# Kernel optimization log

Hardware: AMD Instinct MI355X
Metric: run time of the kernel (lower is better)

## Reference

```python
import jax, jax.numpy as jnp
import numpy as np

N = 100000
E = 1000000
IN_F, HID, NCLS = 128, 128, 40
EPS = 1e-5


def _gconv(h, src, dst, W, b):
    # DGL GraphConv with norm='both', allow_zero_in_degree=True (degrees clamped to >=1).
    ones = jnp.ones(src.shape, jnp.float32)
    dout = jnp.clip(jax.ops.segment_sum(ones, src, num_segments=N), 1.0)   # out-degree of src nodes
    din = jnp.clip(jax.ops.segment_sum(ones, dst, num_segments=N), 1.0)    # in-degree of dst nodes
    x = (h * jax.lax.rsqrt(dout)[:, None]) @ W            # [N, out] matmul-first (linear commutes with sum-aggregation)
    y = jax.ops.segment_sum(x[src], dst, num_segments=N)  # SpMM: scatter-add over edges
    y = y * jax.lax.rsqrt(din)[:, None]
    return y + b if b is not None else y


def _bn(h, gamma, beta):
    # BatchNorm1d training-mode math over the node dimension (biased variance).
    m = jnp.mean(h, axis=0)
    v = jnp.mean(jnp.square(h - m), axis=0)
    return (h - m) * jax.lax.rsqrt(v + EPS) * gamma + beta


def setup_inputs() -> dict:
    key = jax.random.key(0)
    ks = jax.random.split(key, 16)
    feat = jax.random.normal(ks[0], (N, IN_F), jnp.float32)
    src0 = jax.random.randint(ks[1], (E,), 0, N, jnp.int32)
    dst0 = jax.random.randint(ks[2], (E,), 0, N, jnp.int32)
    src1 = jax.random.randint(ks[3], (E,), 0, N, jnp.int32)
    dst1 = jax.random.randint(ks[4], (E,), 0, N, jnp.int32)
    order_attn = jax.random.uniform(ks[5], (2,), jnp.float32)
    s = lambda d_in, d_out: 1.0 / np.sqrt(d_in)
    W0 = jax.random.uniform(ks[6], (IN_F, HID), jnp.float32, -s(IN_F, HID), s(IN_F, HID))
    W1 = jax.random.uniform(ks[7], (HID, HID), jnp.float32, -s(HID, HID), s(HID, HID))
    W2 = jax.random.uniform(ks[8], (HID, NCLS), jnp.float32, -s(HID, NCLS), s(HID, NCLS))
    b2 = jnp.zeros((NCLS,), jnp.float32)
    L0 = jax.random.uniform(ks[9], (IN_F, HID), jnp.float32, -s(IN_F, HID), s(IN_F, HID))
    L1 = jax.random.uniform(ks[10], (HID, HID), jnp.float32, -s(HID, HID), s(HID, HID))
    L2 = jax.random.uniform(ks[11], (HID, NCLS), jnp.float32, -s(HID, NCLS), s(HID, NCLS))
    gamma0 = jnp.ones((HID,), jnp.float32); beta0 = jnp.zeros((HID,), jnp.float32)
    gamma1 = jnp.ones((HID,), jnp.float32); beta1 = jnp.zeros((HID,), jnp.float32)
    return dict(feat=feat, src0=src0, dst0=dst0, src1=src1, dst1=dst1, order_attn=order_attn,
                W0=W0, W1=W1, W2=W2, b2=b2, L0=L0, L1=L1, L2=L2,
                gamma0=gamma0, beta0=beta0, gamma1=gamma1, beta1=beta1)


def reference(feat, src0, dst0, src1, dst1, order_attn, W0, W1, W2, b2, L0, L1, L2,
              gamma0, beta0, gamma1, beta1):
    # Multi-graph path (len(graph)==2, n_layers==3, use_linear=True); dropout = identity (eval).
    h = feat
    # layer 0: order_attn-weighted combination of two adjacency variants
    conv1 = _gconv(h, src0, dst0, W0, None)
    conv2 = _gconv(h, src1, dst1, W0, None)
    conv = order_attn[0] * conv1 + order_attn[1] * conv2
    h = conv + h @ L0
    h = jax.nn.relu(_bn(h, gamma0, beta0))
    # layer 1 (convs[-2]) on graph[0]
    h = _gconv(h, src0, dst0, W1, None) + h @ L1
    h = jax.nn.relu(_bn(h, gamma1, beta1))
    # layer 2 (convs[-1]) on graph[0], with bias
    h = _gconv(h, src0, dst0, W2, b2) + h @ L2
    return h
```

## Files before the change

### kernel.cpp

```cpp
#include <hip/hip_runtime.h>
#include <math.h>

#define N_NODES 100000
#define N_EDGES 1000000
#define F 128
#define NC 40
#define BN_EPS 1e-5f
#define CH 32
#define EC (N_EDGES / CH)
#define WIN0 65536
#define NB1 (N_NODES - WIN0)
#define PROW (N_NODES / 4)
#define CSU 68
#define GB 1563

typedef unsigned int uint;
typedef unsigned short ushort;
typedef __attribute__((ext_vector_type(8))) short vbf8;
typedef __attribute__((ext_vector_type(4))) float vf4;

__device__ __forceinline__ float bf_lo(uint v) { return __uint_as_float(v << 16); }
__device__ __forceinline__ float bf_hi(uint v) { return __uint_as_float(v & 0xffff0000u); }
__device__ __forceinline__ ushort f2bf(float f) {
  uint u = __float_as_uint(f);
  u = u + 0x7fffu + ((u >> 16) & 1u);
  return (ushort)(u >> 16);
}
__device__ __forceinline__ uint pk2(float a, float b) {
  return (uint)f2bf(a) | ((uint)f2bf(b) << 16);
}

__global__ __launch_bounds__(256) void hist_count_k(
    const int* __restrict__ s0, const int* __restrict__ d0,
    const int* __restrict__ s1, const int* __restrict__ d1,
    unsigned* __restrict__ partial) {
  __shared__ unsigned bins[16384];
  int c = blockIdx.x, w = blockIdx.y, a = blockIdx.z;
  const int* keys = (a == 0) ? s0 : (a == 1) ? d0 : (a == 2) ? s1 : d1;
  int base = w * WIN0;
  int nb = w ? NB1 : WIN0;
  int nwords = nb >> 2;
  int t = threadIdx.x;
  for (int i = t; i < nwords; i += 256) bins[i] = 0;
  __syncthreads();
  int e0 = c * EC;
  for (int e = e0 + t; e < e0 + EC; e += 256) {
    int b = keys[e] - base;
    if ((unsigned)b < (unsigned)nb)
      atomicAdd(&bins[b >> 2], 1u << ((b & 3) * 8));
  }
  __syncthreads();
  unsigned* dst = partial + (size_t)(a * CH + c) * PROW + (w ? (WIN0 >> 2) : 0);
  for (int i = t; i < nwords; i += 256) dst[i] = bins[i];
}

__global__ __launch_bounds__(256) void deg_reduce_k(
    unsigned* __restrict__ partial, float* __restrict__ rs4, ushort* __restrict__ rsO01u,
    int* __restrict__ degIn0, int* __restrict__ degIn1) {
  int word = blockIdx.x * 256 + threadIdx.x;
  if (word >= PROW) return;
  int a = blockIdx.y;
  bool din = (a == 1) || (a == 3);
  unsigned r0 = 0, r1 = 0, r2 = 0, r3 = 0;
  unsigned* rowp = partial + (size_t)a * CH * PROW + word;
  for (int c = 0; c < CH; ++c) {
    unsigned* p = rowp + (size_t)c * PROW;
    unsigned v = *p;
    if (din) *p = r0 | (r1 << 8) | (r2 << 16) | (r3 << 24);
    r0 += v & 255u; r1 += (v >> 8) & 255u; r2 += (v >> 16) & 255u; r3 += (v >> 24) & 255u;
  }
  int b = word * 4;
  float4 r;
  r.x = rsqrtf((float)max(r0, 1u));
  r.y = rsqrtf((float)max(r1, 1u));
  r.z = rsqrtf((float)max(r2, 1u));
  r.w = rsqrtf((float)max(r3, 1u));
  *(float4*)&rs4[(size_t)a * N_NODES + b] = r;
  if (a == 0) {
    rsO01u[2 * (b + 0)] = f2bf(r.x); rsO01u[2 * (b + 1)] = f2bf(r.y);
    rsO01u[2 * (b + 2)] = f2bf(r.z); rsO01u[2 * (b + 3)] = f2bf(r.w);
  }
  if (a == 2) {
    rsO01u[2 * (b + 0) + 1] = f2bf(r.x); rsO01u[2 * (b + 1) + 1] = f2bf(r.y);
    rsO01u[2 * (b + 2) + 1] = f2bf(r.z); rsO01u[2 * (b + 3) + 1] = f2bf(r.w);
  }
  if (a == 1) { degIn0[b] = r0; degIn0[b + 1] = r1; degIn0[b + 2] = r2; degIn0[b + 3] = r3; }
  if (a == 3) { degIn1[b] = r0; degIn1[b + 1] = r1; degIn1[b + 2] = r2; degIn1[b + 3] = r3; }
}

__global__ void scan_local_k(const int* __restrict__ cnt0, const int* __restrict__ cnt1,
                             int* __restrict__ out0, int* __restrict__ out1,
                             int* __restrict__ bsum) {
  __shared__ int lds[256];
  const int* cnt = blockIdx.y ? cnt1 : cnt0;
  int* out = blockIdx.y ? out1 : out0;
  int base = blockIdx.x * 2048;
  int t = threadIdx.x;
  int v[8];
  int s = 0;
#pragma unroll
  for (int j = 0; j < 8; ++j) {
    int idx = base + t * 8 + j;
    v[j] = (idx < N_NODES) ? cnt[idx] : 0;
    s += v[j];
  }
  lds[t] = s;
  __syncthreads();
  for (int off = 1; off < 256; off <<= 1) {
    int x = (t >= off) ? lds[t - off] : 0;
    __syncthreads();
    lds[t] += x;
    __syncthreads();
  }
  int excl = lds[t] - s;
  if (t == 255) bsum[blockIdx.y * 64 + blockIdx.x] = lds[255];
  int run = excl;
#pragma unroll
  for (int j = 0; j < 8; ++j) {
    int idx = base + t * 8 + j;
    if (idx < N_NODES) out[idx] = run;
    run += v[j];
  }
}

__global__ void scan_top_k(int* bsum, int nb) {
  int w = threadIdx.x >> 6, t = threadIdx.x & 63;
  int* b = bsum + w * 64;
  int orig = (t < nb) ? b[t] : 0;
  int v = orig;
  for (int off = 1; off < 64; off <<= 1) {
    int u = __shfl_up(v, off);
    if (t >= off) v += u;
  }
  if (t < nb) b[t] = v - orig;
}

__global__ void scan_apply_k(int* __restrict__ rp0, int* __restrict__ rp1,
                             const int* __restrict__ bsum) {
  int* rp = blockIdx.y ? rp1 : rp0;
  const int* bs = bsum + blockIdx.y * 64;
  int i = blockIdx.x * 256 + threadIdx.x;
  if (i < N_NODES) rp[i] += bs[i >> 11];
  if (i == 0) rp[N_NODES] = N_EDGES;
}

__global__ __launch_bounds__(256) void csr_fill2_k(
    const int* __restrict__ src0, const int* __restrict__ dst0, const int* __restrict__ rp0g,
    int* __restrict__ csr0g,
    const int* __restrict__ src1, const int* __restrict__ dst1, const int* __restrict__ rp1g,
    int* __restrict__ csr1g, const unsigned* __restrict__ partial) {
  __shared__ unsigned bins[16384];
  int c = blockIdx.x, w = blockIdx.y, g = blockIdx.z;
  const int* src = g ? src1 : src0;
  const int* dst = g ? dst1 : dst0;
  const int* rp = g ? rp1g : rp0g;
  int* csr = g ? csr1g : csr0g;
  int aIdx = g ? 3 : 1;
  int base = w * WIN0;
  int nb = w ? NB1 : WIN0;
  int nwords = nb >> 2;
  const unsigned* sp = partial + (size_t)(aIdx * CH + c) * PROW + (w ? (WIN0 >> 2) : 0);
  int t = threadIdx.x;
  for (int i = t; i < nwords; i += 256) bins[i] = sp[i];
  __syncthreads();
  int e0 = c * EC;
  for (int e = e0 + t; e < e0 + EC; e += 256) {
    int d = dst[e];
    int b = d - base;
    if ((unsigned)b < (unsigned)nb) {
      int sh = (b & 3) * 8;
      unsigned old = atomicAdd(&bins[b >> 2], 1u << sh);
      int off = (old >> sh) & 255;
      csr[rp[d] + off] = src[e];
    }
  }
}

__global__ __launch_bounds__(256) void pack_all_k(
    const float* __restrict__ x, uint* __restrict__ y,
    const float* __restrict__ Wa, const float* __restrict__ Wb,
    const float* __restrict__ Wc, const float* __restrict__ Wd,
    ushort* __restrict__ pk) {
  int b = blockIdx.x;
  int t = threadIdx.x;
  if (b < 1024) {
    size_t total = (size_t)N_NODES * F / 8;
    for (size_t idx = b * 256 + t; idx < total; idx += (size_t)1024 * 256) {
      float4 v1 = ((const float4*)x)[idx * 2];
      float4 v2 = ((const float4*)x)[idx * 2 + 1];
      uint4 o;
      o.x = pk2(v1.x, v1.y);
      o.y = pk2(v1.z, v1.w);
      o.z = pk2(v2.x, v2.y);
      o.w = pk2(v2.z, v2.w);
      ((uint4*)y)[idx] = o;
    }
  } else {
    int bb = b - 1024;
    int m = bb >> 3;
    int idx = (bb & 7) * 256 + t;
    const float* W = (m == 0) ? Wa : (m == 1) ? Wb : (m == 2) ? Wc : Wd;
    int lane = idx & 63;
    int nt = (idx >> 6) & 7;
    int ks = idx >> 9;
    int j = (lane & 15) + nt * 16;
    int kb = (lane >> 4) * 8 + ks * 32;
    ushort v[8];
#pragma unroll
    for (int q = 0; q < 8; ++q) v[q] = f2bf(W[(size_t)(kb + q) * F + j]);
    *(uint4*)(pk + (size_t)m * 16384 + (size_t)idx * 8) = *(uint4*)v;
  }
}

__global__ void st_part_k(const float* __restrict__ stm, float* __restrict__ stp, int ncopies) {
  int b = blockIdx.x, t = threadIdx.x;
  int lo = b * 25, hi = min(ncopies, lo + 25);
  float s = 0.f;
  for (int k = lo; k < hi; ++k) s += stm[(size_t)k * 256 + t];
  stp[b * 256 + t] = s;
}

__global__ void st_final_k(const float* __restrict__ stp, float* __restrict__ st) {
  int t = threadIdx.x;
  float s = 0.f;
#pragma unroll
  for (int k = 0; k < 64; ++k) s += stp[k * 256 + t];
  st[t] = s;
}

__device__ __forceinline__ void acc8(uint4 v, float c, float* a) {
  a[0] = fmaf(bf_lo(v.x), c, a[0]); a[1] = fmaf(bf_hi(v.x), c, a[1]);
  a[2] = fmaf(bf_lo(v.y), c, a[2]); a[3] = fmaf(bf_hi(v.y), c, a[3]);
  a[4] = fmaf(bf_lo(v.z), c, a[4]); a[5] = fmaf(bf_hi(v.z), c, a[5]);
  a[6] = fmaf(bf_lo(v.w), c, a[6]); a[7] = fmaf(bf_hi(v.w), c, a[7]);
}

__device__ __forceinline__ void gather_run(const int* __restrict__ p, int n, float w,
                                           const float* __restrict__ rsO,
                                           const uint4* __restrict__ xr, int l, float* a) {
  int e = 0;
  for (; e + 3 < n; e += 4) {
    int s0 = p[e], s1 = p[e + 1], s2 = p[e + 2], s3 = p[e + 3];
    float c0 = w * rsO[s0], c1 = w * rsO[s1];
    float c2 = w * rsO[s2], c3 = w * rsO[s3];
    uint4 v0 = xr[(size_t)s0 * 16 + l];
    uint4 v1 = xr[(size_t)s1 * 16 + l];
    uint4 v2 = xr[(size_t)s2 * 16 + l];
    uint4 v3 = xr[(size_t)s3 * 16 + l];
    acc8(v0, c0, a); acc8(v1, c1, a); acc8(v2, c2, a); acc8(v3, c3, a);
  }
  for (; e < n; ++e) {
    int s = p[e];
    float c = w * rsO[s];
    uint4 v = xr[(size_t)s * 16 + l];
    acc8(v, c, a);
  }
}

__global__ __launch_bounds__(256) void gather_dual_q_k(
    const uint* __restrict__ xbf, const float* __restrict__ attn,
    const float* __restrict__ rsO0f, const float* __restrict__ rsO1f,
    const float* __restrict__ rsI0, const int* __restrict__ rp0, const int* __restrict__ csr0,
    const float* __restrict__ rsI1, const int* __restrict__ rp1, const int* __restrict__ csr1,
    uint* __restrict__ outbf) {
  int node = blockIdx.x * 16 + (threadIdx.x >> 4);
  int l = threadIdx.x & 15;
  int b0 = rp0[node], n0 = rp0[node + 1] - b0;
  int b1 = rp1[node], n1 = rp1[node + 1] - b1;
  float w0 = attn[0] * rsI0[node];
  float w1 = attn[1] * rsI1[node];
  const uint4* xr = (const uint4*)xbf;
  float a[8] = {0.f, 0.f, 0.f, 0.f, 0.f, 0.f, 0.f, 0.f};
  gather_run(csr0 + b0, n0, w0, rsO0f, xr, l, a);
  gather_run(csr1 + b1, n1, w1, rsO1f, xr, l, a);
  uint4 o;
  o.x = pk2(a[0], a[1]); o.y = pk2(a[2], a[3]);
  o.z = pk2(a[4], a[5]); o.w = pk2(a[6], a[7]);
  ((uint4*)outbf)[(size_t)node * 16 + l] = o;
}

__device__ __forceinline__ void accbn(uint4 v, float c, const float* sc, const float* sh,
                                      float* a) {
  a[0] = fmaf(fmaxf(fmaf(bf_lo(v.x), sc[0], sh[0]), 0.f), c, a[0]);
  a[1] = fmaf(fmaxf(fmaf(bf_hi(v.x), sc[1], sh[1]), 0.f), c, a[1]);
  a[2] = fmaf(fmaxf(fmaf(bf_lo(v.y), sc[2], sh[2]), 0.f), c, a[2]);
  a[3] = fmaf(fmaxf(fmaf(bf_hi(v.y), sc[3], sh[3]), 0.f), c, a[3]);
  a[4] = fmaf(fmaxf(fmaf(bf_lo(v.z), sc[4], sh[4]), 0.f), c, a[4]);
  a[5] = fmaf(fmaxf(fmaf(bf_hi(v.z), sc[5], sh[5]), 0.f), c, a[5]);
  a[6] = fmaf(fmaxf(fmaf(bf_lo(v.w), sc[6], sh[6]), 0.f), c, a[6]);
  a[7] = fmaf(fmaxf(fmaf(bf_hi(v.w), sc[7], sh[7]), 0.f), c, a[7]);
}

__global__ __launch_bounds__(256) void gather_bn_q_k(
    const uint* __restrict__ xbf, const float* __restrict__ st,
    const float* __restrict__ gamma, const float* __restrict__ beta,
    const float* __restrict__ rsO,
    const float* __restrict__ rsI, const int* __restrict__ rp, const int* __restrict__ csr,
    uint* __restrict__ outbf) {
  int node = blockIdx.x * 16 + (threadIdx.x >> 4);
  int l = threadIdx.x & 15;
  float sc[8], sh[8];
#pragma unroll
  for (int j = 0; j < 8; ++j) {
    int c = 8 * l + j;
    float m = st[c] * (1.f / (float)N_NODES);
    float v = st[128 + c] * (1.f / (float)N_NODES) - m * m;
    float s = gamma[c] * rsqrtf(fmaxf(v, 0.f) + BN_EPS);
    sc[j] = s;
    sh[j] = beta[c] - m * s;
  }
  int b0 = rp[node], T = rp[node + 1] - b0;
  const int* p = csr + b0;
  const uint4* xr = (const uint4*)xbf;
  float a[8] = {0.f, 0.f, 0.f, 0.f, 0.f, 0.f, 0.f, 0.f};
  int e = 0;
  for (; e + 1 < T; e += 2) {
    int s0 = p[e], s1 = p[e + 1];
    float c0 = rsO[s0], c1 = rsO[s1];
    uint4 v0 = xr[(size_t)s0 * 16 + l];
    uint4 v1 = xr[(size_t)s1 * 16 + l];
    accbn(v0, c0, sc, sh, a);
    accbn(v1, c1, sc, sh, a);
  }
  if (e < T) {
    int s0 = p[e];
    float c0 = rsO[s0];
    uint4 v0 = xr[(size_t)s0 * 16 + l];
    accbn(v0, c0, sc, sh, a);
  }
  float sd = rsI[node];
  uint4 o;
  o.x = pk2(a[0] * sd, a[1] * sd); o.y = pk2(a[2] * sd, a[3] * sd);
  o.z = pk2(a[4] * sd, a[5] * sd); o.w = pk2(a[6] * sd, a[7] * sd);
  ((uint4*)outbf)[(size_t)node * 16 + l] = o;
}

__global__ void gather40_add_k(const uint* __restrict__ x2bf, const float* __restrict__ rsI,
                               const int* __restrict__ rp, const int* __restrict__ csr,
                               float* __restrict__ out) {
  int node = (blockIdx.x * 256 + threadIdx.x) >> 5;
  int lane = threadIdx.x & 31;
  if (node >= N_NODES || lane >= 20) return;
  float l = 0.f, h = 0.f;
  int e = rp[node], end = rp[node + 1];
  for (; e + 3 < end; e += 4) {
    int sA = csr[e], sB = csr[e + 1], sC = csr[e + 2], sD = csr[e + 3];
    uint vA = x2bf[(size_t)sA * 20 + lane];
    uint vB = x2bf[(size_t)sB * 20 + lane];
    uint vC = x2bf[(size_t)sC * 20 + lane];
    uint vD = x2bf[(size_t)sD * 20 + lane];
    l += (bf_lo(vA) + bf_lo(vB)) + (bf_lo(vC) + bf_lo(vD));
    h += (bf_hi(vA) + bf_hi(vB)) + (bf_hi(vC) + bf_hi(vD));
  }
  for (; e < end; ++e) {
    uint vA = x2bf[(size_t)csr[e] * 20 + lane];
    l += bf_lo(vA);
    h += bf_hi(vA);
  }
  float sd = rsI[node];
  float2 p = *(float2*)(out + (size_t)node * NC + lane * 2);
  *(float2*)(out + (size_t)node * NC + lane * 2) = make_float2(p.x + l * sd, p.y + h * sd);
}

__global__ __launch_bounds__(256) void gemm_mfma_k(
    const ushort* __restrict__ A1, const ushort* __restrict__ A2,
    const ushort* __restrict__ pkA, const ushort* __restrict__ pkB,
    float* __restrict__ stm, ushort* __restrict__ Cb) {
  __shared__ uint Cl[64 * CSU];
  __shared__ float sst[256];
  int t = threadIdx.x;
  sst[t] = 0.f;
  __syncthreads();
  int wave = t >> 6, lane = t & 63;
  int kgrp = lane >> 4, lrow = lane & 15;
  int arow = blockIdx.x * 64 + wave * 16 + lrow;
  bool rok = arow < N_NODES;
  const vbf8* a1p = (const vbf8*)(A1 + (size_t)(rok ? arow : 0) * F);
  const vbf8* a2p = (const vbf8*)(A2 + (size_t)(rok ? arow : 0) * F);
  const vbf8* wap = (const vbf8*)pkA + lane;
  const vbf8* wbp = (const vbf8*)pkB + lane;
  vbf8 zero = {0, 0, 0, 0, 0, 0, 0, 0};
  vf4 acc[8];
#pragma unroll
  for (int i = 0; i < 8; ++i) acc[i] = (vf4){0.f, 0.f, 0.f, 0.f};
#pragma unroll
  for (int ks = 0; ks < 4; ++ks) {
    vbf8 a1 = rok ? a1p[ks * 4 + kgrp] : zero;
    vbf8 a2 = rok ? a2p[ks * 4 + kgrp] : zero;
#pragma unroll
    for (int nt = 0; nt < 8; ++nt)
      acc[nt] = __builtin_amdgcn_mfma_f32_16x16x32_bf16(a1, wap[(ks * 8 + nt) * 64], acc[nt], 0, 0, 0);
#pragma unroll
    for (int nt = 0; nt < 8; ++nt)
      acc[nt] = __builtin_amdgcn_mfma_f32_16x16x32_bf16(a2, wbp[(ks * 8 + nt) * 64], acc[nt], 0, 0, 0);
  }
  int row_l = wave * 16 + kgrp * 4;
#pragma unroll
  for (int nt = 0; nt < 8; ++nt) {
#pragma unroll
    for (int r = 0; r < 4; ++r) {
      float w = acc[nt][r];
      float o = __shfl_xor(w, 1);
      if ((lrow & 1) == 0) Cl[(row_l + r) * CSU + nt * 8 + (lrow >> 1)] = pk2(w, o);
    }
  }
#pragma unroll
  for (int nt = 0; nt < 8; ++nt) {
    float s = acc[nt][0] + acc[nt][1] + acc[nt][2] + acc[nt][3];
    float q = acc[nt][0] * acc[nt][0] + acc[nt][1] * acc[nt][1] +
              acc[nt][2] * acc[nt][2] + acc[nt][3] * acc[nt][3];
    s += __shfl_xor(s, 16); q += __shfl_xor(q, 16);
    s += __shfl_xor(s, 32); q += __shfl_xor(q, 32);
    if (lane < 16) {
      atomicAdd(&sst[nt * 16 + lane], s);
      atomicAdd(&sst[128 + nt * 16 + lane], q);
    }
  }
  __syncthreads();
#pragma unroll
  for (int i = 0; i < 4; ++i) {
    int u = t + 256 * i;
    int row = u >> 4, seg = (u & 15) * 4;
    int grow = blockIdx.x * 64 + row;
    if (grow < N_NODES)
      *(uint4*)((uint*)Cb + (size_t)grow * 64 + seg) = *(uint4*)&Cl[row * CSU + seg];
  }
  stm[(size_t)blockIdx.x * 256 + t] = sst[t];
}

__global__ __launch_bounds__(256) void gemm_mfma_bn_k(
    const ushort* __restrict__ A1, const ushort* __restrict__ A2,
    const float* __restrict__ stin, const float* __restrict__ gamma,
    const float* __restrict__ beta,
    const ushort* __restrict__ pkA, const ushort* __restrict__ pkB,
    float* __restrict__ stm, ushort* __restrict__ Cb) {
  __shared__ uint Cl[64 * CSU];
  __shared__ float sst[256];
  __shared__ float scl[128], shl[128];
  int t = threadIdx.x;
  sst[t] = 0.f;
  if (t < 128) {
    float m = stin[t] * (1.f / (float)N_NODES);
    float v = stin[128 + t] * (1.f / (float)N_NODES) - m * m;
    float s = gamma[t] * rsqrtf(fmaxf(v, 0.f) + BN_EPS);
    scl[t] = s;
    shl[t] = beta[t] - m * s;
  }
  __syncthreads();
  int wave = t >> 6, lane = t & 63;
  int kgrp = lane >> 4, lrow = lane & 15;
  int arow = blockIdx.x * 64 + wave * 16 + lrow;
  bool rok = arow < N_NODES;
  const vbf8* a1p = (const vbf8*)(A1 + (size_t)(rok ? arow : 0) * F);
  const vbf8* a2p = (const vbf8*)(A2 + (size_t)(rok ? arow : 0) * F);
  const vbf8* wap = (const vbf8*)pkA + lane;
  const vbf8* wbp = (const vbf8*)pkB + lane;
  vbf8 zero = {0, 0, 0, 0, 0, 0, 0, 0};
  vf4 acc[8];
#pragma unroll
  for (int i = 0; i < 8; ++i) acc[i] = (vf4){0.f, 0.f, 0.f, 0.f};
#pragma unroll
  for (int ks = 0; ks < 4; ++ks) {
    vbf8 a1 = rok ? a1p[ks * 4 + kgrp] : zero;
    vbf8 a2 = zero;
    if (rok) {
      vbf8 a2r = a2p[ks * 4 + kgrp];
      const float* scp = &scl[ks * 32 + kgrp * 8];
      const float* shp = &shl[ks * 32 + kgrp * 8];
      ushort o[8];
#pragma unroll
      for (int q = 0; q < 8; ++q) {
        float f = __uint_as_float(((uint)(ushort)a2r[q]) << 16);
        f = fmaxf(fmaf(f, scp[q], shp[q]), 0.f);
        o[q] = f2bf(f);
      }
      a2 = *(vbf8*)o;
    }
#pragma unroll
    for (int nt = 0; nt < 8; ++nt)
      acc[nt] = __builtin_amdgcn_mfma_f32_16x16x32_bf16(a1, wap[(ks * 8 + nt) * 64], acc[nt], 0, 0, 0);
#pragma unroll
    for (int nt = 0; nt < 8; ++nt)
      acc[nt] = __builtin_amdgcn_mfma_f32_16x16x32_bf16(a2, wbp[(ks * 8 + nt) * 64], acc[nt], 0, 0, 0);
  }
  int row_l = wave * 16 + kgrp * 4;
#pragma unroll
  for (int nt = 0; nt < 8; ++nt) {
#pragma unroll
    for (int r = 0; r < 4; ++r) {
      float w = acc[nt][r];
      float o = __shfl_xor(w, 1);
      if ((lrow & 1) == 0) Cl[(row_l + r) * CSU + nt * 8 + (lrow >> 1)] = pk2(w, o);
    }
  }
#pragma unroll
  for (int nt = 0; nt < 8; ++nt) {
    float s = acc[nt][0] + acc[nt][1] + acc[nt][2] + acc[nt][3];
    float q = acc[nt][0] * acc[nt][0] + acc[nt][1] * acc[nt][1] +
              acc[nt][2] * acc[nt][2] + acc[nt][3] * acc[nt][3];
    s += __shfl_xor(s, 16); q += __shfl_xor(q, 16);
    s += __shfl_xor(s, 32); q += __shfl_xor(q, 32);
    if (lane < 16) {
      atomicAdd(&sst[nt * 16 + lane], s);
      atomicAdd(&sst[128 + nt * 16 + lane], q);
    }
  }
  __syncthreads();
#pragma unroll
  for (int i = 0; i < 4; ++i) {
    int u = t + 256 * i;
    int row = u >> 4, seg = (u & 15) * 4;
    int grow = blockIdx.x * 64 + row;
    if (grow < N_NODES)
      *(uint4*)((uint*)Cb + (size_t)grow * 64 + seg) = *(uint4*)&Cl[row * CSU + seg];
  }
  stm[(size_t)blockIdx.x * 256 + t] = sst[t];
}

__global__ __launch_bounds__(256) void gemm40_dual_k(
    const uint* __restrict__ h1b, const float* __restrict__ st,
    const float* __restrict__ gamma, const float* __restrict__ beta,
    const float* __restrict__ W2, const float* __restrict__ L2, const float* __restrict__ bias,
    const float* __restrict__ rsO, uint* __restrict__ x2bf, float* __restrict__ outp) {
  __shared__ float Alds[25 * 128];
  __shared__ float Wl[128 * NC];
  __shared__ float Ll[128 * NC];
  __shared__ float scl[128], shl[128];
  int t = threadIdx.x;
  int r0 = blockIdx.x * 25;
  if (t < 128) {
    float m = st[t] / (float)N_NODES;
    float v = st[128 + t] / (float)N_NODES - m * m;
    float s = gamma[t] * rsqrtf(fmaxf(v, 0.f) + BN_EPS);
    scl[t] = s;
    shl[t] = beta[t] - m * s;
  }
  __syncthreads();
#pragma unroll
  for (int p = 0; p < 4; ++p) {
    int flat = t * 4 + p * 1024;
    if (flat < 25 * 128) {
      int lrr = flat >> 7, k = flat & 127;
      int row = r0 + lrr;
      float4 v = make_float4(0.f, 0.f, 0.f, 0.f);
      if (row < N_NODES) {
        uint2 u = *(const uint2*)(h1b + (size_t)row * 64 + (k >> 1));
        v = make_float4(bf_lo(u.x), bf_hi(u.x), bf_lo(u.y), bf_hi(u.y));
      }
      float4 scv = *(float4*)&scl[k];
      float4 shv = *(float4*)&shl[k];
      v.x = fmaxf(fmaf(v.x, scv.x, shv.x), 0.f);
      v.y = fmaxf(fmaf(v.y, scv.y, shv.y), 0.f);
      v.z = fmaxf(fmaf(v.z, scv.z, shv.z), 0.f);
      v.w = fmaxf(fmaf(v.w, scv.w, shv.w), 0.f);
      *(float4*)&Alds[flat] = v;
    }
  }
#pragma unroll
  for (int p = 0; p < 5; ++p) {
    int flat = t * 4 + p * 1024;
    if (flat < 128 * NC) {
      *(float4*)&Wl[flat] = *(const float4*)(W2 + flat);
      *(float4*)&Ll[flat] = *(const float4*)(L2 + flat);
    }
  }
  __syncthreads();
  if (t < 250) {
    int lrr = t / 10, cg = t % 10;
    float w0 = 0.f, w1 = 0.f, w2 = 0.f, w3 = 0.f;
    float l0 = 0.f, l1 = 0.f, l2 = 0.f, l3 = 0.f;
#pragma unroll 8
    for (int k = 0; k < 128; ++k) {
      float a = Alds[lrr * 128 + k];
      float4 w = *(float4*)&Wl[k * NC + cg * 4];
      float4 l = *(float4*)&Ll[k * NC + cg * 4];
      w0 = fmaf(a, w.x, w0); w1 = fmaf(a, w.y, w1);
      w2 = fmaf(a, w.z, w2); w3 = fmaf(a, w.w, w3);
      l0 = fmaf(a, l.x, l0); l1 = fmaf(a, l.y, l1);
      l2 = fmaf(a, l.z, l2); l3 = fmaf(a, l.w, l3);
    }
    int row = r0 + lrr;
    if (row < N_NODES) {
      float s = rsO[row];
      uint2 xo = make_uint2(pk2(w0 * s, w1 * s), pk2(w2 * s, w3 * s));
      *(uint2*)(x2bf + (size_t)row * 20 + cg * 2) = xo;
      float4 bv = *(const float4*)(bias + cg * 4);
      float4 oo = make_float4(l0 + bv.x, l1 + bv.y, l2 + bv.z, l3 + bv.w);
      *(float4*)(outp + (size_t)row * NC + cg * 4) = oo;
    }
  }
}

extern "C" void kernel_launch(void* const* d_in, const int* in_sizes, int n_in,
                              void* d_out, int out_size, void* d_ws, size_t ws_size,
                              hipStream_t stream) {
  const float* feat = (const float*)d_in[0];
  const int* src0 = (const int*)d_in[1];
  const int* dst0 = (const int*)d_in[2];
  const int* src1 = (const int*)d_in[3];
  const int* dst1 = (const int*)d_in[4];
  const float* attn = (const float*)d_in[5];
  const float* W0 = (const float*)d_in[6];
  const float* W1 = (const float*)d_in[7];
  const float* W2 = (const float*)d_in[8];
  const float* b2 = (const float*)d_in[9];
  const float* L0 = (const float*)d_in[10];
  const float* L1 = (const float*)d_in[11];
  const float* L2 = (const float*)d_in[12];
  const float* gamma0 = (const float*)d_in[13];
  const float* beta0 = (const float*)d_in[14];
  const float* gamma1 = (const float*)d_in[15];
  const float* beta1 = (const float*)d_in[16];
  float* out = (float*)d_out;

  char* base = (char*)d_ws;
  size_t off = 0;
  auto alloc = [&](size_t bytes) -> void* {
    void* p = base + off;
    off += (bytes + 255) & ~(size_t)255;
    return p;
  };
  unsigned* partial = (unsigned*)alloc((size_t)4 * CH * PROW * 4);
  float* rs4 = (float*)alloc(4 * (size_t)N_NODES * 4);
  uint* rsO01 = (uint*)alloc((size_t)N_NODES * 4);
  int* degIn0 = (int*)alloc(N_NODES * 4);
  int* degIn1 = (int*)alloc(N_NODES * 4);
  int* rp0 = (int*)alloc((N_NODES + 1) * 4);
  int* rp1 = (int*)alloc((N_NODES + 1) * 4);
  int* bsum = (int*)alloc(128 * 4);
  int* csr0 = (int*)alloc((size_t)N_EDGES * 4);
  int* csr1 = (int*)alloc((size_t)N_EDGES * 4);
  float* stm0 = (float*)alloc((size_t)GB * 256 * 4);
  float* stm1 = (float*)alloc((size_t)GB * 256 * 4);
  float* stp = (float*)alloc((size_t)64 * 256 * 4);
  float* st0 = (float*)alloc(256 * 4);
  float* st1 = (float*)alloc(256 * 4);
  ushort* wpk = (ushort*)alloc((size_t)4 * 16384 * 2);
  uint* featbf = (uint*)alloc((size_t)N_NODES * 64 * 4);
  uint* aggbf = (uint*)alloc((size_t)N_NODES * 64 * 4);
  uint* hrow = (uint*)alloc((size_t)N_NODES * 64 * 4);
  uint* g1buf = (uint*)alloc((size_t)N_NODES * 64 * 4);
  if (off > ws_size) return;

  uint* x2bf = featbf;

  float* rs_out0 = rs4;
  float* rs_in0 = rs4 + N_NODES;
  float* rs_out1 = rs4 + 2 * N_NODES;
  float* rs_in1 = rs4 + 3 * N_NODES;

  hist_count_k<<<dim3(CH, 2, 4), 256, 0, stream>>>(src0, dst0, src1, dst1, partial);
  deg_reduce_k<<<dim3((PROW + 255) / 256, 4), 256, 0, stream>>>(
      partial, rs4, (ushort*)rsO01, degIn0, degIn1);
  const int SCB = (N_NODES + 2047) / 2048;
  scan_local_k<<<dim3(SCB, 2), 256, 0, stream>>>(degIn0, degIn1, rp0, rp1, bsum);
  scan_top_k<<<1, 128, 0, stream>>>(bsum, SCB);
  scan_apply_k<<<dim3((N_NODES + 255) / 256, 2), 256, 0, stream>>>(rp0, rp1, bsum);
  csr_fill2_k<<<dim3(CH, 2, 2), 256, 0, stream>>>(src0, dst0, rp0, csr0,
                                                  src1, dst1, rp1, csr1, partial);

  pack_all_k<<<1056, 256, 0, stream>>>(feat, featbf, W0, L0, W1, L1, wpk);

  gather_dual_q_k<<<N_NODES / 16, 256, 0, stream>>>(featbf, attn, rs_out0, rs_out1,
                                                    rs_in0, rp0, csr0,
                                                    rs_in1, rp1, csr1, aggbf);
  gemm_mfma_k<<<GB, 256, 0, stream>>>((ushort*)aggbf, (ushort*)featbf, wpk, wpk + 16384,
                                      stm0, (ushort*)hrow);
  st_part_k<<<64, 256, 0, stream>>>(stm0, stp, GB);
  st_final_k<<<1, 256, 0, stream>>>(stp, st0);

  gather_bn_q_k<<<N_NODES / 16, 256, 0, stream>>>(hrow, st0, gamma0, beta0, rs_out0,
                                                  rs_in0, rp0, csr0, g1buf);
  gemm_mfma_bn_k<<<GB, 256, 0, stream>>>((ushort*)g1buf, (ushort*)hrow, st0, gamma0, beta0,
                                         wpk + 2 * 16384, wpk + 3 * 16384, stm1, (ushort*)hrow);
  st_part_k<<<64, 256, 0, stream>>>(stm1, stp, GB);
  st_final_k<<<1, 256, 0, stream>>>(stp, st1);

  gemm40_dual_k<<<(N_NODES + 24) / 25, 256, 0, stream>>>(hrow, st1, gamma1, beta1, W2, L2, b2,
                                                         rs_out0, x2bf, out);
  gather40_add_k<<<(N_NODES * 32 + 255) / 256, 256, 0, stream>>>(x2bf, rs_in0, rp0, csr0, out);
}
```

Baseline: 468.1 us.

## Split 128-wide gathers into eight 16-feature column slices across grid.x

The two 128-feature SpMM gather kernels now run over a 2D grid where blockIdx.x picks a 16-column slice and each node uses 4 lanes loading uint2, instead of 16 lanes loading uint4 over the full row. Blocks working on the same slice touch only a 3.2 MB portion of the feature matrix, so the random gathers are meant to hit in L2/MALL more often. The cost is that each node's CSR indices and degree scales are re-read eight times. The dual gather also reads the packed bf16 rsO01 out-degree scales instead of two fp32 arrays, which lowers coefficient precision slightly.

Result: slower. 721.4 us (+54.1%).

```diff
diff --git a/kernel.cpp b/kernel.cpp
--- a/kernel.cpp
+++ b/kernel.cpp
@@ -228,111 +228,136 @@
   st[t] = s;
 }
 
-__device__ __forceinline__ void acc8(uint4 v, float c, float* a) {
-  a[0] = fmaf(bf_lo(v.x), c, a[0]); a[1] = fmaf(bf_hi(v.x), c, a[1]);
-  a[2] = fmaf(bf_lo(v.y), c, a[2]); a[3] = fmaf(bf_hi(v.y), c, a[3]);
-  a[4] = fmaf(bf_lo(v.z), c, a[4]); a[5] = fmaf(bf_hi(v.z), c, a[5]);
-  a[6] = fmaf(bf_lo(v.w), c, a[6]); a[7] = fmaf(bf_hi(v.w), c, a[7]);
-}
-
-__device__ __forceinline__ void gather_run(const int* __restrict__ p, int n, float w,
-                                           const float* __restrict__ rsO,
-                                           const uint4* __restrict__ xr, int l, float* a) {
-  int e = 0;
-  for (; e + 3 < n; e += 4) {
-    int s0 = p[e], s1 = p[e + 1], s2 = p[e + 2], s3 = p[e + 3];
-    float c0 = w * rsO[s0], c1 = w * rsO[s1];
-    float c2 = w * rsO[s2], c3 = w * rsO[s3];
-    uint4 v0 = xr[(size_t)s0 * 16 + l];
-    uint4 v1 = xr[(size_t)s1 * 16 + l];
-    uint4 v2 = xr[(size_t)s2 * 16 + l];
-    uint4 v3 = xr[(size_t)s3 * 16 + l];
-    acc8(v0, c0, a); acc8(v1, c1, a); acc8(v2, c2, a); acc8(v3, c3, a);
-  }
-  for (; e < n; ++e) {
-    int s = p[e];
-    float c = w * rsO[s];
-    uint4 v = xr[(size_t)s * 16 + l];
-    acc8(v, c, a);
-  }
-}
-
-__global__ __launch_bounds__(256) void gather_dual_q_k(
+__global__ __launch_bounds__(256) void gather_dual_s_k(
     const uint* __restrict__ xbf, const float* __restrict__ attn,
-    const float* __restrict__ rsO0f, const float* __restrict__ rsO1f,
+    const uint* __restrict__ rsO01,
     const float* __restrict__ rsI0, const int* __restrict__ rp0, const int* __restrict__ csr0,
     const float* __restrict__ rsI1, const int* __restrict__ rp1, const int* __restrict__ csr1,
     uint* __restrict__ outbf) {
-  int node = blockIdx.x * 16 + (threadIdx.x >> 4);
-  int l = threadIdx.x & 15;
+  int s = blockIdx.x;
+  int node = blockIdx.y * 64 + (threadIdx.x >> 2);
+  int sl = threadIdx.x & 3;
+  if (node >= N_NODES) return;
+  const uint2* xc = (const uint2*)xbf + s * 4 + sl;
   int b0 = rp0[node], n0 = rp0[node + 1] - b0;
   int b1 = rp1[node], n1 = rp1[node + 1] - b1;
   float w0 = attn[0] * rsI0[node];
   float w1 = attn[1] * rsI1[node];
-  const uint4* xr = (const uint4*)xbf;
-  float a[8] = {0.f, 0.f, 0.f, 0.f, 0.f, 0.f, 0.f, 0.f};
-  gather_run(csr0 + b0, n0, w0, rsO0f, xr, l, a);
-  gather_run(csr1 + b1, n1, w1, rsO1f, xr, l, a);
-  uint4 o;
-  o.x = pk2(a[0], a[1]); o.y = pk2(a[2], a[3]);
-  o.z = pk2(a[4], a[5]); o.w = pk2(a[6], a[7]);
-  ((uint4*)outbf)[(size_t)node * 16 + l] = o;
-}
-
-__device__ __forceinline__ void accbn(uint4 v, float c, const float* sc, const float* sh,
-                                      float* a) {
-  a[0] = fmaf(fmaxf(fmaf(bf_lo(v.x), sc[0], sh[0]), 0.f), c, a[0]);
-  a[1] = fmaf(fmaxf(fmaf(bf_hi(v.x), sc[1], sh[1]), 0.f), c, a[1]);
-  a[2] = fmaf(fmaxf(fmaf(bf_lo(v.y), sc[2], sh[2]), 0.f), c, a[2]);
-  a[3] = fmaf(fmaxf(fmaf(bf_hi(v.y), sc[3], sh[3]), 0.f), c, a[3]);
-  a[4] = fmaf(fmaxf(fmaf(bf_lo(v.z), sc[4], sh[4]), 0.f), c, a[4]);
-  a[5] = fmaf(fmaxf(fmaf(bf_hi(v.z), sc[5], sh[5]), 0.f), c, a[5]);
-  a[6] = fmaf(fmaxf(fmaf(bf_lo(v.w), sc[6], sh[6]), 0.f), c, a[6]);
-  a[7] = fmaf(fmaxf(fmaf(bf_hi(v.w), sc[7], sh[7]), 0.f), c, a[7]);
-}
-
-__global__ __launch_bounds__(256) void gather_bn_q_k(
+  float a0 = 0.f, a1 = 0.f, a2 = 0.f, a3 = 0.f;
+  {
+    const int* p = csr0 + b0;
+    int e = 0;
+    for (; e + 3 < n0; e += 4) {
+      int s0 = p[e], s1 = p[e + 1], s2 = p[e + 2], s3 = p[e + 3];
+      float c0 = w0 * bf_lo(rsO01[s0]);
+      float c1 = w0 * bf_lo(rsO01[s1]);
+      float c2 = w0 * bf_lo(rsO01[s2]);
+      float c3 = w0 * bf_lo(rsO01[s3]);
+      uint2 v0 = xc[(size_t)s0 * 32];
+      uint2 v1 = xc[(size_t)s1 * 32];
+      uint2 v2 = xc[(size_t)s2 * 32];
+      uint2 v3 = xc[(size_t)s3 * 32];
+      a0 = fmaf(bf_lo(v0.x), c0, a0); a1 = fmaf(bf_hi(v0.x), c0, a1);
+      a2 = fmaf(bf_lo(v0.y), c0, a2); a3 = fmaf(bf_hi(v0.y), c0, a3);
+      a0 = fmaf(bf_lo(v1.x), c1, a0); a1 = fmaf(bf_hi(v1.x), c1, a1);
+      a2 = fmaf(bf_lo(v1.y), c1, a2); a3 = fmaf(bf_hi(v1.y), c1, a3);
+      a0 = fmaf(bf_lo(v2.x), c2, a0); a1 = fmaf(bf_hi(v2.x), c2, a1);
+      a2 = fmaf(bf_lo(v2.y), c2, a2); a3 = fmaf(bf_hi(v2.y), c2, a3);
+      a0 = fmaf(bf_lo(v3.x), c3, a0); a1 = fmaf(bf_hi(v3.x), c3, a1);
+      a2 = fmaf(bf_lo(v3.y), c3, a2); a3 = fmaf(bf_hi(v3.y), c3, a3);
+    }
+    for (; e < n0; ++e) {
+      int s0 = p[e];
+      float c0 = w0 * bf_lo(rsO01[s0]);
+      uint2 v0 = xc[(size_t)s0 * 32];
+      a0 = fmaf(bf_lo(v0.x), c0, a0); a1 = fmaf(bf_hi(v0.x), c0, a1);
+      a2 = fmaf(bf_lo(v0.y), c0, a2); a3 = fmaf(bf_hi(v0.y), c0, a3);
+    }
+  }
+  {
+    const int* p = csr1 + b1;
+    int e = 0;
+    for (; e + 3 < n1; e += 4) {
+      int s0 = p[e], s1 = p[e + 1], s2 = p[e + 2], s3 = p[e + 3];
+      float c0 = w1 * bf_hi(rsO01[s0]);
+      float c1 = w1 * bf_hi(rsO01[s1]);
+      float c2 = w1 * bf_hi(rsO01[s2]);
+      float c3 = w1 * bf_hi(rsO01[s3]);
+      uint2 v0 = xc[(size_t)s0 * 32];
+      uint2 v1 = xc[(size_t)s1 * 32];
+      uint2 v2 = xc[(size_t)s2 * 32];
+      uint2 v3 = xc[(size_t)s3 * 32];
+      a0 = fmaf(bf_lo(v0.x), c0, a0); a1 = fmaf(bf_hi(v0.x), c0, a1);
+      a2 = fmaf(bf_lo(v0.y), c0, a2); a3 = fmaf(bf_hi(v0.y), c0, a3);
+      a0 = fmaf(bf_lo(v1.x), c1, a0); a1 = fmaf(bf_hi(v1.x), c1, a1);
+      a2 = fmaf(bf_lo(v1.y), c1, a2); a3 = fmaf(bf_hi(v1.y), c1, a3);
+      a0 = fmaf(bf_lo(v2.x), c2, a0); a1 = fmaf(bf_hi(v2.x), c2, a1);
+      a2 = fmaf(bf_lo(v2.y), c2, a2); a3 = fmaf(bf_hi(v2.y), c2, a3);
+      a0 = fmaf(bf_lo(v3.x), c3, a0); a1 = fmaf(bf_hi(v3.x), c3, a1);
+      a2 = fmaf(bf_lo(v3.y), c3, a2); a3 = fmaf(bf_hi(v3.y), c3, a3);
+    }
+    for (; e < n1; ++e) {
+      int s0 = p[e];
+      float c0 = w1 * bf_hi(rsO01[s0]);
+      uint2 v0 = xc[(size_t)s0 * 32];
+      a0 = fmaf(bf_lo(v0.x), c0, a0); a1 = fmaf(bf_hi(v0.x), c0, a1);
+      a2 = fmaf(bf_lo(v0.y), c0, a2); a3 = fmaf(bf_hi(v0.y), c0, a3);
+    }
+  }
+  ((uint2*)outbf)[(size_t)node * 32 + s * 4 + sl] = make_uint2(pk2(a0, a1), pk2(a2, a3));
+}
+
+__global__ __launch_bounds__(256) void gather_bn_s_k(
     const uint* __restrict__ xbf, const float* __restrict__ st,
     const float* __restrict__ gamma, const float* __restrict__ beta,
     const float* __restrict__ rsO,
     const float* __restrict__ rsI, const int* __restrict__ rp, const int* __restrict__ csr,
     uint* __restrict__ outbf) {
-  int node = blockIdx.x * 16 + (threadIdx.x >> 4);
-  int l = threadIdx.x & 15;
-  float sc[8], sh[8];
-#pragma unroll
-  for (int j = 0; j < 8; ++j) {
-    int c = 8 * l + j;
+  int s = blockIdx.x;
+  int node = blockIdx.y * 64 + (threadIdx.x >> 2);
+  int sl = threadIdx.x & 3;
+  if (node >= N_NODES) return;
+  float sc[4], sh[4];
+#pragma unroll
+  for (int j = 0; j < 4; ++j) {
+    int c = s * 16 + sl * 4 + j;
     float m = st[c] * (1.f / (float)N_NODES);
     float v = st[128 + c] * (1.f / (float)N_NODES) - m * m;
-    float s = gamma[c] * rsqrtf(fmaxf(v, 0.f) + BN_EPS);
-    sc[j] = s;
-    sh[j] = beta[c] - m * s;
-  }
+    float g = gamma[c] * rsqrtf(fmaxf(v, 0.f) + BN_EPS);
+    sc[j] = g;
+    sh[j] = beta[c] - m * g;
+  }
+  const uint2* xc = (const uint2*)xbf + s * 4 + sl;
   int b0 = rp[node], T = rp[node + 1] - b0;
   const int* p = csr + b0;
-  const uint4* xr = (const uint4*)xbf;
-  float a[8] = {0.f, 0.f, 0.f, 0.f, 0.f, 0.f, 0.f, 0.f};
+  float a0 = 0.f, a1 = 0.f, a2 = 0.f, a3 = 0.f;
   int e = 0;
   for (; e + 1 < T; e += 2) {
     int s0 = p[e], s1 = p[e + 1];
     float c0 = rsO[s0], c1 = rsO[s1];
-    uint4 v0 = xr[(size_t)s0 * 16 + l];
-    uint4 v1 = xr[(size_t)s1 * 16 + l];
-    accbn(v0, c0, sc, sh, a);
-    accbn(v1, c1, sc, sh, a);
+    uint2 v0 = xc[(size_t)s0 * 32];
+    uint2 v1 = xc[(size_t)s1 * 32];
+    a0 = fmaf(fmaxf(fmaf(bf_lo(v0.x), sc[0], sh[0]), 0.f), c0, a0);
+    a1 = fmaf(fmaxf(fmaf(bf_hi(v0.x), sc[1], sh[1]), 0.f), c0, a1);
+    a2 = fmaf(fmaxf(fmaf(bf_lo(v0.y), sc[2], sh[2]), 0.f), c0, a2);
+    a3 = fmaf(fmaxf(fmaf(bf_hi(v0.y), sc[3], sh[3]), 0.f), c0, a3);
+    a0 = fmaf(fmaxf(fmaf(bf_lo(v1.x), sc[0], sh[0]), 0.f), c1, a0);
+    a1 = fmaf(fmaxf(fmaf(bf_hi(v1.x), sc[1], sh[1]), 0.f), c1, a1);
+    a2 = fmaf(fmaxf(fmaf(bf_lo(v1.y), sc[2], sh[2]), 0.f), c1, a2);
+    a3 = fmaf(fmaxf(fmaf(bf_hi(v1.y), sc[3], sh[3]), 0.f), c1, a3);
   }
   if (e < T) {
     int s0 = p[e];
     float c0 = rsO[s0];
-    uint4 v0 = xr[(size_t)s0 * 16 + l];
-    accbn(v0, c0, sc, sh, a);
+    uint2 v0 = xc[(size_t)s0 * 32];
+    a0 = fmaf(fmaxf(fmaf(bf_lo(v0.x), sc[0], sh[0]), 0.f), c0, a0);
+    a1 = fmaf(fmaxf(fmaf(bf_hi(v0.x), sc[1], sh[1]), 0.f), c0, a1);
+    a2 = fmaf(fmaxf(fmaf(bf_lo(v0.y), sc[2], sh[2]), 0.f), c0, a2);
+    a3 = fmaf(fmaxf(fmaf(bf_hi(v0.y), sc[3], sh[3]), 0.f), c0, a3);
   }
   float sd = rsI[node];
-  uint4 o;
-  o.x = pk2(a[0] * sd, a[1] * sd); o.y = pk2(a[2] * sd, a[3] * sd);
-  o.z = pk2(a[4] * sd, a[5] * sd); o.w = pk2(a[6] * sd, a[7] * sd);
-  ((uint4*)outbf)[(size_t)node * 16 + l] = o;
+  ((uint2*)outbf)[(size_t)node * 32 + s * 4 + sl] =
+      make_uint2(pk2(a0 * sd, a1 * sd), pk2(a2 * sd, a3 * sd));
 }
 
 __global__ void gather40_add_k(const uint* __restrict__ x2bf, const float* __restrict__ rsI,
@@ -661,7 +686,9 @@
 
   pack_all_k<<<1056, 256, 0, stream>>>(feat, featbf, W0, L0, W1, L1, wpk);
 
-  gather_dual_q_k<<<N_NODES / 16, 256, 0, stream>>>(featbf, attn, rs_out0, rs_out1,
+  const int GYB = (N_NODES + 63) / 64;
+
+  gather_dual_s_k<<<dim3(8, GYB), 256, 0, stream>>>(featbf, attn, rsO01,
                                                     rs_in0, rp0, csr0,
                                                     rs_in1, rp1, csr1, aggbf);
   gemm_mfma_k<<<GB, 256, 0, stream>>>((ushort*)aggbf, (ushort*)featbf, wpk, wpk + 16384,
@@ -669,7 +696,7 @@
   st_part_k<<<64, 256, 0, stream>>>(stm0, stp, GB);
   st_final_k<<<1, 256, 0, stream>>>(stp, st0);
 
-  gather_bn_q_k<<<N_NODES / 16, 256, 0, stream>>>(hrow, st0, gamma0, beta0, rs_out0,
+  gather_bn_s_k<<<dim3(8, GYB), 256, 0, stream>>>(hrow, st0, gamma0, beta0, rs_out0,
                                                   rs_in0, rp0, csr0, g1buf);
   gemm_mfma_bn_k<<<GB, 256, 0, stream>>>((ushort*)g1buf, (ushort*)hrow, st0, gamma0, beta0,
                                          wpk + 2 * 16384, wpk + 3 * 16384, stm1, (ushort*)hrow);
```
